# Optimization experiments

Measured on AMD Instinct MI355X. Metric: run time of the kernel, lower is better.

## Reference

```python
import jax, jax.numpy as jnp
import numpy as np

LSTM_IN = 125
LSTM_H = 125
MLP_D_H = 512
N = 512


def _lstm_scan(x, Wih, Whh, bih, bhh):
    # x: (N, LSTM_IN); PyTorch gate order: i, f, g, o
    H = LSTM_H
    def step(carry, xt):
        h, c = carry
        g = Wih @ xt + Whh @ h + bih + bhh  # (4H,)
        i = jax.nn.sigmoid(g[:H])
        f = jax.nn.sigmoid(g[H:2 * H])
        gg = jnp.tanh(g[2 * H:3 * H])
        o = jax.nn.sigmoid(g[3 * H:])
        c = f * c + i * gg
        h = o * jnp.tanh(c)
        return (h, c), h
    init = (jnp.zeros((H,), x.dtype), jnp.zeros((H,), x.dtype))
    _, hs = jax.lax.scan(step, init, x)
    return hs  # (N, H)


def setup_inputs() -> dict:
    key = jax.random.key(0)
    ks = jax.random.split(key, 14)
    s = 0.05
    d = {
        "sentence_emb": jax.random.normal(ks[0], (N, 1, LSTM_IN), jnp.float32),
        "Wih_f": jax.random.normal(ks[1], (4 * LSTM_H, LSTM_IN), jnp.float32) * s,
        "Whh_f": jax.random.normal(ks[2], (4 * LSTM_H, LSTM_H), jnp.float32) * s,
        "bih_f": jax.random.normal(ks[3], (4 * LSTM_H,), jnp.float32) * s,
        "bhh_f": jax.random.normal(ks[4], (4 * LSTM_H,), jnp.float32) * s,
        "Wih_b": jax.random.normal(ks[5], (4 * LSTM_H, LSTM_IN), jnp.float32) * s,
        "Whh_b": jax.random.normal(ks[6], (4 * LSTM_H, LSTM_H), jnp.float32) * s,
        "bih_b": jax.random.normal(ks[7], (4 * LSTM_H,), jnp.float32) * s,
        "bhh_b": jax.random.normal(ks[8], (4 * LSTM_H,), jnp.float32) * s,
        "W1": jax.random.normal(ks[9], (MLP_D_H, 4 * LSTM_H), jnp.float32) * s,
        "b1": jax.random.normal(ks[10], (MLP_D_H,), jnp.float32) * s,
        "W2": jax.random.normal(ks[11], (1, MLP_D_H), jnp.float32) * s,
        "b2": jax.random.normal(ks[12], (1,), jnp.float32) * s,
    }
    return d


def reference(sentence_emb, Wih_f, Whh_f, bih_f, bhh_f, Wih_b, Whh_b, bih_b, bhh_b, W1, b1, W2, b2):
    x = sentence_emb[:, 0, :]  # (N, 125), batch=1
    h_fwd = _lstm_scan(x, Wih_f, Whh_f, bih_f, bhh_f)           # (N, 125)
    h_bwd = _lstm_scan(x[::-1], Wih_b, Whh_b, bih_b, bhh_b)[::-1]  # (N, 125)
    h = jnp.concatenate([h_fwd, h_bwd], axis=-1)  # (N, 250)
    # output_mtx[i, j] = MLP(concat(h[j], h[i]))
    # Decompose first linear: W1 @ cat(h_j, h_i) = Wa @ h_j + Wb @ h_i
    D = h.shape[-1]
    Pa = h @ W1[:, :D].T   # (N, H): contribution of h_j
    Pb = h @ W1[:, D:].T   # (N, H): contribution of h_i
    hidden = jnp.tanh(Pb[:, None, :] + Pa[None, :, :] + b1)  # (N, N, H)
    out = hidden @ W2[0] + b2[0]  # (N, N)
    return out
```

## Files before the change

### kernel.cpp

```cpp
#include <hip/hip_runtime.h>

typedef __bf16 bf16_t;
typedef __bf16 bf16x8 __attribute__((ext_vector_type(8)));
typedef float f32x4 __attribute__((ext_vector_type(4)));
typedef int   int4v __attribute__((ext_vector_type(4)));

#define LOG2E 1.4426950408889634f

template<int CTRL>
__device__ __forceinline__ float qperm(float x) {
  return __builtin_bit_cast(float,
      __builtin_amdgcn_update_dpp(0, __builtin_bit_cast(int, x), CTRL, 0xF, 0xF, true));
}

__device__ __forceinline__ void lds_barrier() {
  asm volatile("s_waitcnt lgkmcnt(0)\n\ts_barrier" ::: "memory");
}

__global__ __launch_bounds__(256) void pre_kernel(
    const float* __restrict__ x,
    const float* __restrict__ Wih_f, const float* __restrict__ bih_f,
    const float* __restrict__ bhh_f,
    const float* __restrict__ Wih_b, const float* __restrict__ bih_b,
    const float* __restrict__ bhh_b,
    float* __restrict__ preT)
{
  const int dir = blockIdx.x >> 5;
  const int T   = blockIdx.x & 31;
  const float* __restrict__ Wih = dir ? Wih_b : Wih_f;
  const float* __restrict__ bih = dir ? bih_b : bih_f;
  const float* __restrict__ bhh = dir ? bhh_b : bhh_f;

  const int tid = threadIdx.x;
  const int wv  = tid >> 6;
  const int lane = tid & 63;
  const int q = lane >> 4, cc = lane & 15;

  const int r  = 16 * T + cc;
  const int na = r >> 2, pa = r & 3;
  const bool vld = (na < 125);
  const float* __restrict__ Wr = Wih + (vld ? (125 * pa + na) * 125 : 0);

  bf16x8 whi[4], wlo[4];
  #pragma unroll
  for (int ks = 0; ks < 4; ++ks) {
    #pragma unroll
    for (int j = 0; j < 8; ++j) {
      int k = 32 * ks + 8 * q + j;
      float wvv = (vld && k < 125) ? Wr[k] : 0.0f;
      bf16_t hi = (bf16_t)wvv;
      whi[ks][j] = hi;
      wlo[ks][j] = (bf16_t)(wvv - (float)hi);
    }
  }

  float bias[4];
  #pragma unroll
  for (int reg = 0; reg < 4; ++reg) {
    int ro = 16 * T + 4 * q + reg;
    int no = ro >> 2, po = ro & 3;
    bias[reg] = (no < 125) ? (bih[125 * po + no] + bhh[125 * po + no]) : 0.0f;
  }

  for (int i = 0; i < 8; ++i) {
    const int tt = 8 * wv + i;
    const int t  = 16 * tt + cc;
    const int trow = dir ? (511 - t) : t;
    const float* __restrict__ xr = x + trow * 125;

    f32x4 acc = (f32x4)0.0f;
    #pragma unroll
    for (int ks = 0; ks < 4; ++ks) {
      bf16x8 xhi, xlo;
      #pragma unroll
      for (int j = 0; j < 8; ++j) {
        int k = 32 * ks + 8 * q + j;
        float xv = (k < 125) ? xr[k] : 0.0f;
        bf16_t hi = (bf16_t)xv;
        xhi[j] = hi;
        xlo[j] = (bf16_t)(xv - (float)hi);
      }
      acc = __builtin_amdgcn_mfma_f32_16x16x32_bf16(whi[ks], xhi, acc, 0, 0, 0);
      acc = __builtin_amdgcn_mfma_f32_16x16x32_bf16(whi[ks], xlo, acc, 0, 0, 0);
      acc = __builtin_amdgcn_mfma_f32_16x16x32_bf16(wlo[ks], xhi, acc, 0, 0, 0);
    }
    #pragma unroll
    for (int reg = 0; reg < 4; ++reg) {
      int ro = 16 * T + 4 * q + reg;
      preT[dir * 262144 + ro * 512 + 16 * tt + cc] = acc[reg] + bias[reg];
    }
  }
}

__global__ __launch_bounds__(512) void lstm_kernel(
    const float* __restrict__ Whh_f, const float* __restrict__ Whh_b,
    const float* __restrict__ pre,
    bf16_t* __restrict__ h_all)
{
  const int dir = blockIdx.x;
  const float* __restrict__ Whh = dir ? Whh_b : Whh_f;

  const int tid  = threadIdx.x;
  const int lane = tid & 63;
  const int w    = tid >> 6;
  const int q    = lane >> 4;
  const int cc   = lane & 15;
  const int lt   = cc >> 2;
  const int p    = cc & 3;

  float wm = 0.0f;
  #pragma unroll
  for (int LT = 0; LT < 4; ++LT) {
    int rr = 16 * (4 * w + LT) + cc;
    int nn = rr >> 2, pp = rr & 3;
    if (nn < 125) {
      const float* __restrict__ Wrow = Whh + (125 * pp + nn) * 125;
      #pragma unroll
      for (int ks = 0; ks < 2; ++ks)
        #pragma unroll
        for (int jj = 0; jj < 16; ++jj) {
          int k = 64 * ks + 16 * q + jj;
          if (k < 125) wm = fmaxf(wm, fabsf(Wrow[k]));
        }
    }
  }
  #pragma unroll
  for (int off = 1; off < 64; off <<= 1)
    wm = fmaxf(wm, __shfl_xor(wm, off));
  __shared__ float wmx[8];
  if (lane == 0) wmx[w] = wm;
  __syncthreads();
  float wmax = wmx[0];
  #pragma unroll
  for (int u = 1; u < 8; ++u) wmax = fmaxf(wmax, wmx[u]);
  const float s_w  = 127.0f / wmax;
  const float invq = wmax / (127.0f * 127.0f);

  int4v afrag[4][2];
  #pragma unroll
  for (int LT = 0; LT < 4; ++LT) {
    int rr = 16 * (4 * w + LT) + cc;
    int nn = rr >> 2, pp = rr & 3;
    bool avld = (nn < 125);
    const float* __restrict__ Wrow = Whh + (avld ? (125 * pp + nn) * 125 : 0);
    #pragma unroll
    for (int ks = 0; ks < 2; ++ks) {
      int4v v;
      #pragma unroll
      for (int word = 0; word < 4; ++word) {
        int b = 0;
        #pragma unroll
        for (int byte = 0; byte < 4; ++byte) {
          int jj = 4 * word + byte;
          int k  = 64 * ks + 16 * q + jj;
          int qv = 0;
          if (avld && k < 125)
            qv = (int)__builtin_rintf(Wrow[k] * s_w);
          b |= (qv & 0xFF) << (8 * byte);
        }
        v[word] = b;
      }
      afrag[LT][ks] = v;
    }
  }

  __shared__ __align__(16) char hbuf[2][128];
  if (tid < 256) hbuf[tid >> 7][tid & 127] = 0;
  if (dir == 0) {
    #pragma unroll
    for (int u = 0; u < 6; ++u) h_all[tid * 256 + 250 + u] = (bf16_t)0.0f;
  }
  __syncthreads();

  const int   r_lane = 64 * w + 16 * lt + 4 * q + p;
  const int   nset   = 16 * w + 4 * lt + q;
  const float mult   = (p == 2) ? (-2.0f * LOG2E) : (-LOG2E);
  const float sA     = (p == 2) ? 2.0f : 1.0f;
  const float sB     = (p == 2) ? -1.0f : 0.0f;
  const float dscale = mult * invq;
  const float* __restrict__ preR = pre + dir * 262144 + r_lane * 512;
  float c = 0.0f;

  float4 pv_cur = *(const float4*)preR;

  for (int g = 0; g < 128; ++g) {
    float4 pv_nxt = make_float4(0.f, 0.f, 0.f, 0.f);
    if (g < 127) pv_nxt = *(const float4*)(preR + 4 * (g + 1));

    #pragma unroll
    for (int s4 = 0; s4 < 4; ++s4) {
      const int step = 4 * g + s4;
      const int cur  = s4 & 1, nxt = cur ^ 1;
      const float pv = (s4 == 0) ? pv_cur.x : (s4 == 1) ? pv_cur.y
                     : (s4 == 2) ? pv_cur.z : pv_cur.w;
      const float pvm = mult * pv;

      int4v b0 = *(const int4v*)&hbuf[cur][16 * q];
      int4v b1 = *(const int4v*)&hbuf[cur][64 + 16 * q];

      int4v acc[4];
      #pragma unroll
      for (int LT = 0; LT < 4; ++LT) {
        int4v a = (int4v)0;
        a = __builtin_amdgcn_mfma_i32_16x16x64_i8(afrag[LT][0], b0, a, 0, 0, 0);
        a = __builtin_amdgcn_mfma_i32_16x16x64_i8(afrag[LT][1], b1, a, 0, 0, 0);
        acc[LT] = a;
      }

      int gl[4];
      #pragma unroll
      for (int LT = 0; LT < 4; ++LT) {
        int a01 = (p & 1) ? acc[LT][1] : acc[LT][0];
        int a23 = (p & 1) ? acc[LT][3] : acc[LT][2];
        gl[LT] = (p & 2) ? a23 : a01;
      }
      int b01 = (lt & 1) ? gl[1] : gl[0];
      int b23 = (lt & 1) ? gl[3] : gl[2];
      int gsel = (lt & 2) ? b23 : b01;

      float gf  = (float)gsel;
      float xg  = fmaf(gf, dscale, pvm);
      float e   = __builtin_amdgcn_exp2f(xg);
      float y   = __builtin_amdgcn_rcpf(1.0f + e);
      float act = fmaf(y, sA, sB);

      float b_i = qperm<0x00>(act);
      float b_f = qperm<0x55>(act);
      float b_g = qperm<0xAA>(act);
      float b_o = qperm<0xFF>(act);
      c = fmaf(b_f, c, b_i * b_g);
      float e2 = __builtin_amdgcn_exp2f(-2.0f * LOG2E * c);
      float tc = fmaf(__builtin_amdgcn_rcpf(1.0f + e2), 2.0f, -1.0f);
      float h  = b_o * tc;

      if (p == 0) {
        int qh = (int)__builtin_rintf(h * 127.0f);
        hbuf[nxt][nset] = (char)qh;
        if (nset < 125) {
          int t_orig = dir ? (511 - step) : step;
          h_all[t_orig * 256 + dir * 125 + nset] = (bf16_t)h;
        }
      }
      lds_barrier();
    }
    pv_cur = pv_nxt;
  }
}

__global__ __launch_bounds__(256) void qgemm_kernel(
    const bf16_t* __restrict__ h_all,
    const float* __restrict__ W1,
    const float* __restrict__ b1,
    float* __restrict__ Qa,
    float* __restrict__ Qb)
{
  const int tid  = threadIdx.x;
  const int wv   = tid >> 6;
  const int lane = tid & 63;
  const int q    = lane >> 4, cc = lane & 15;
  const int bj   = blockIdx.x & 31;
  const int bm   = blockIdx.x >> 5;
  const int m    = bm * 64 + wv * 16 + cc;
  const int j0   = bj * 16;
  const int jA   = j0 + cc;

  const bool isB = (m >= 512);
  const int  row = isB ? (m - 512) : m;
  const int  cof = isB ? 250 : 0;

  f32x4 acc = (f32x4)0.0f;
  #pragma unroll
  for (int ks = 0; ks < 8; ++ks) {
    int kb = 32 * ks + 8 * q;
    bf16x8 a = *(const bf16x8*)&h_all[jA * 256 + kb];
    bf16x8 b;
    #pragma unroll
    for (int jj = 0; jj < 8; ++jj) {
      int k = kb + jj;
      float v = (k < 250) ? W1[row * 500 + cof + k] : 0.0f;
      b[jj] = (bf16_t)v;
    }
    acc = __builtin_amdgcn_mfma_f32_16x16x32_bf16(a, b, acc, 0, 0, 0);
  }

  const float C2 = 2.0f * LOG2E;
  #pragma unroll
  for (int reg = 0; reg < 4; ++reg) {
    int j = j0 + 4 * q + reg;
    float v = acc[reg];
    if (!isB) Qa[j * 512 + m] = C2 * v;
    else      Qb[j * 512 + (m - 512)] = C2 * (v + b1[m - 512]);
  }
}

__global__ __launch_bounds__(256) void outer_kernel(
    const float* __restrict__ Qa, const float* __restrict__ Qb,
    const float* __restrict__ W2, const float* __restrict__ b2,
    float* __restrict__ out)
{
  __shared__ float sa[2][32][33];
  __shared__ float sb[2][32][33];
  __shared__ float sw[2][32];

  const int tid = threadIdx.x;
  const int bi  = blockIdx.x >> 4, bjx = blockIdx.x & 15;
  const int i0  = bi * 32, j0 = bjx * 32;
  const int ii0 = (tid & 15) * 2;
  const int jj0 = (tid >> 4) * 2;
  const int ljj = tid & 31, kk4 = (tid >> 5) * 4;

  float accR[2][2] = {{0.0f, 0.0f}, {0.0f, 0.0f}};
  float wsum = 0.0f;

  for (int kc = 0; kc < 16; ++kc) {
    const int buf = kc & 1;
    const int k0  = kc * 32;
    float4 va = *(const float4*)&Qa[(j0 + ljj) * 512 + k0 + kk4];
    float4 vb = *(const float4*)&Qb[(i0 + ljj) * 512 + k0 + kk4];
    sa[buf][kk4 + 0][ljj] = va.x; sa[buf][kk4 + 1][ljj] = va.y;
    sa[buf][kk4 + 2][ljj] = va.z; sa[buf][kk4 + 3][ljj] = va.w;
    sb[buf][kk4 + 0][ljj] = vb.x; sb[buf][kk4 + 1][ljj] = vb.y;
    sb[buf][kk4 + 2][ljj] = vb.z; sb[buf][kk4 + 3][ljj] = vb.w;
    if (tid < 32) sw[buf][tid] = W2[k0 + tid];
    __syncthreads();

    #pragma unroll 4
    for (int kk = 0; kk < 32; ++kk) {
      float2 av = *(const float2*)&sa[buf][kk][jj0];
      float2 bv = *(const float2*)&sb[buf][kk][ii0];
      float wk = sw[buf][kk];
      wsum += wk;
      {
        float e = __builtin_amdgcn_exp2f(av.x + bv.x);
        accR[0][0] = fmaf(wk, __builtin_amdgcn_rcpf(1.0f + e), accR[0][0]);
      }
      {
        float e = __builtin_amdgcn_exp2f(av.y + bv.x);
        accR[0][1] = fmaf(wk, __builtin_amdgcn_rcpf(1.0f + e), accR[0][1]);
      }
      {
        float e = __builtin_amdgcn_exp2f(av.x + bv.y);
        accR[1][0] = fmaf(wk, __builtin_amdgcn_rcpf(1.0f + e), accR[1][0]);
      }
      {
        float e = __builtin_amdgcn_exp2f(av.y + bv.y);
        accR[1][1] = fmaf(wk, __builtin_amdgcn_rcpf(1.0f + e), accR[1][1]);
      }
    }
  }

  const float bb = b2[0];
  #pragma unroll
  for (int i2 = 0; i2 < 2; ++i2)
    #pragma unroll
    for (int j2 = 0; j2 < 2; ++j2)
      out[(i0 + ii0 + i2) * 512 + (j0 + jj0 + j2)] =
          wsum - 2.0f * accR[i2][j2] + bb;
}

extern "C" void kernel_launch(void* const* d_in, const int* in_sizes, int n_in,
                              void* d_out, int out_size, void* d_ws, size_t ws_size,
                              hipStream_t stream) {
  const float* emb   = (const float*)d_in[0];
  const float* Wih_f = (const float*)d_in[1];
  const float* Whh_f = (const float*)d_in[2];
  const float* bih_f = (const float*)d_in[3];
  const float* bhh_f = (const float*)d_in[4];
  const float* Wih_b = (const float*)d_in[5];
  const float* Whh_b = (const float*)d_in[6];
  const float* bih_b = (const float*)d_in[7];
  const float* bhh_b = (const float*)d_in[8];
  const float* W1    = (const float*)d_in[9];
  const float* b1    = (const float*)d_in[10];
  const float* W2    = (const float*)d_in[11];
  const float* b2    = (const float*)d_in[12];
  float* out = (float*)d_out;

  char* ws = (char*)d_ws;
  float*  pre   = (float*)ws;
  bf16_t* h_all = (bf16_t*)(ws + 2 * 1024 * 1024);
  float*  Qa    = (float*)(ws + 2 * 1024 * 1024 + 256 * 1024);
  float*  Qb    = Qa + 512 * 512;

  pre_kernel<<<64, 256, 0, stream>>>(emb, Wih_f, bih_f, bhh_f,
                                     Wih_b, bih_b, bhh_b, pre);
  lstm_kernel<<<2, 512, 0, stream>>>(Whh_f, Whh_b, pre, h_all);
  qgemm_kernel<<<512, 256, 0, stream>>>(h_all, W1, b1, Qa, Qb);
  outer_kernel<<<256, 256, 0, stream>>>(Qa, Qb, W2, b2, out);
}
```

Measured before the change: 336.3 us.

## Replace per-step int8 MFMA recurrent matvec with per-thread sdot4 dot products

```diff
diff --git a/kernel.cpp b/kernel.cpp
--- a/kernel.cpp
+++ b/kernel.cpp
@@ -16,6 +16,19 @@
 __device__ __forceinline__ void lds_barrier() {
   asm volatile("s_waitcnt lgkmcnt(0)\n\ts_barrier" ::: "memory");
 }
+
+#if __has_builtin(__builtin_amdgcn_sdot4)
+__device__ __forceinline__ int DOT4(int a, int b, int c) {
+  return __builtin_amdgcn_sdot4(a, b, c, false);
+}
+#else
+__device__ __forceinline__ int DOT4(int a, int b, int c) {
+  #pragma unroll
+  for (int i = 0; i < 4; ++i)
+    c += ((a << (24 - 8 * i)) >> 24) * ((b << (24 - 8 * i)) >> 24);
+  return c;
+}
+#endif
 
 __global__ __launch_bounds__(256) void pre_kernel(
     const float* __restrict__ x,
@@ -103,27 +116,23 @@
   const int tid  = threadIdx.x;
   const int lane = tid & 63;
   const int w    = tid >> 6;
-  const int q    = lane >> 4;
-  const int cc   = lane & 15;
-  const int lt   = cc >> 2;
-  const int p    = cc & 3;
-
-  float wm = 0.0f;
-  #pragma unroll
-  for (int LT = 0; LT < 4; ++LT) {
-    int rr = 16 * (4 * w + LT) + cc;
-    int nn = rr >> 2, pp = rr & 3;
-    if (nn < 125) {
-      const float* __restrict__ Wrow = Whh + (125 * pp + nn) * 125;
-      #pragma unroll
-      for (int ks = 0; ks < 2; ++ks)
-        #pragma unroll
-        for (int jj = 0; jj < 16; ++jj) {
-          int k = 64 * ks + 16 * q + jj;
-          if (k < 125) wm = fmaxf(wm, fabsf(Wrow[k]));
-        }
-    }
-  }
+  const int n    = tid >> 2;
+  const int p    = tid & 3;
+  const bool vld = (n < 125);
+  const float* __restrict__ Wrow = Whh + (vld ? (125 * p + n) * 125 : 0);
+
+  float m0 = 0.f, m1 = 0.f, m2 = 0.f, m3 = 0.f;
+  if (vld) {
+    #pragma unroll 4
+    for (int k = 0; k < 124; k += 4) {
+      m0 = fmaxf(m0, fabsf(Wrow[k + 0]));
+      m1 = fmaxf(m1, fabsf(Wrow[k + 1]));
+      m2 = fmaxf(m2, fabsf(Wrow[k + 2]));
+      m3 = fmaxf(m3, fabsf(Wrow[k + 3]));
+    }
+    m0 = fmaxf(m0, fabsf(Wrow[124]));
+  }
+  float wm = fmaxf(fmaxf(m0, m1), fmaxf(m2, m3));
   #pragma unroll
   for (int off = 1; off < 64; off <<= 1)
     wm = fmaxf(wm, __shfl_xor(wm, off));
@@ -136,49 +145,34 @@
   const float s_w  = 127.0f / wmax;
   const float invq = wmax / (127.0f * 127.0f);
 
-  int4v afrag[4][2];
-  #pragma unroll
-  for (int LT = 0; LT < 4; ++LT) {
-    int rr = 16 * (4 * w + LT) + cc;
-    int nn = rr >> 2, pp = rr & 3;
-    bool avld = (nn < 125);
-    const float* __restrict__ Wrow = Whh + (avld ? (125 * pp + nn) * 125 : 0);
-    #pragma unroll
-    for (int ks = 0; ks < 2; ++ks) {
-      int4v v;
-      #pragma unroll
-      for (int word = 0; word < 4; ++word) {
-        int b = 0;
-        #pragma unroll
-        for (int byte = 0; byte < 4; ++byte) {
-          int jj = 4 * word + byte;
-          int k  = 64 * ks + 16 * q + jj;
-          int qv = 0;
-          if (avld && k < 125)
-            qv = (int)__builtin_rintf(Wrow[k] * s_w);
-          b |= (qv & 0xFF) << (8 * byte);
-        }
-        v[word] = b;
-      }
-      afrag[LT][ks] = v;
-    }
+  int wq[32];
+  #pragma unroll
+  for (int word = 0; word < 32; ++word) {
+    int b = 0;
+    #pragma unroll
+    for (int byte = 0; byte < 4; ++byte) {
+      int k = 4 * word + byte;
+      int qv = 0;
+      if (vld && k < 125)
+        qv = (int)__builtin_rintf(Wrow[k] * s_w);
+      b |= (qv & 0xFF) << (8 * byte);
+    }
+    wq[word] = b;
   }
 
   __shared__ __align__(16) char hbuf[2][128];
-  if (tid < 256) hbuf[tid >> 7][tid & 127] = 0;
+  if (tid < 256) ((char*)hbuf)[tid] = 0;
   if (dir == 0) {
     #pragma unroll
     for (int u = 0; u < 6; ++u) h_all[tid * 256 + 250 + u] = (bf16_t)0.0f;
   }
   __syncthreads();
 
-  const int   r_lane = 64 * w + 16 * lt + 4 * q + p;
-  const int   nset   = 16 * w + 4 * lt + q;
   const float mult   = (p == 2) ? (-2.0f * LOG2E) : (-LOG2E);
   const float sA     = (p == 2) ? 2.0f : 1.0f;
   const float sB     = (p == 2) ? -1.0f : 0.0f;
   const float dscale = mult * invq;
-  const float* __restrict__ preR = pre + dir * 262144 + r_lane * 512;
+  const float* __restrict__ preR = pre + dir * 262144 + tid * 512;
   float c = 0.0f;
 
   float4 pv_cur = *(const float4*)preR;
@@ -195,30 +189,27 @@
                      : (s4 == 2) ? pv_cur.z : pv_cur.w;
       const float pvm = mult * pv;
 
-      int4v b0 = *(const int4v*)&hbuf[cur][16 * q];
-      int4v b1 = *(const int4v*)&hbuf[cur][64 + 16 * q];
-
-      int4v acc[4];
+      int hv[32];
       #pragma unroll
-      for (int LT = 0; LT < 4; ++LT) {
-        int4v a = (int4v)0;
-        a = __builtin_amdgcn_mfma_i32_16x16x64_i8(afrag[LT][0], b0, a, 0, 0, 0);
-        a = __builtin_amdgcn_mfma_i32_16x16x64_i8(afrag[LT][1], b1, a, 0, 0, 0);
-        acc[LT] = a;
-      }
-
-      int gl[4];
+      for (int j = 0; j < 8; ++j) {
+        int4v v = *(const int4v*)&hbuf[cur][16 * j];
+        hv[4 * j + 0] = v[0];
+        hv[4 * j + 1] = v[1];
+        hv[4 * j + 2] = v[2];
+        hv[4 * j + 3] = v[3];
+      }
+
+      int d0 = 0, d1 = 0, d2 = 0, d3 = 0;
       #pragma unroll
-      for (int LT = 0; LT < 4; ++LT) {
-        int a01 = (p & 1) ? acc[LT][1] : acc[LT][0];
-        int a23 = (p & 1) ? acc[LT][3] : acc[LT][2];
-        gl[LT] = (p & 2) ? a23 : a01;
-      }
-      int b01 = (lt & 1) ? gl[1] : gl[0];
-      int b23 = (lt & 1) ? gl[3] : gl[2];
-      int gsel = (lt & 2) ? b23 : b01;
-
-      float gf  = (float)gsel;
+      for (int j = 0; j < 8; ++j) {
+        d0 = DOT4(wq[4 * j + 0], hv[4 * j + 0], d0);
+        d1 = DOT4(wq[4 * j + 1], hv[4 * j + 1], d1);
+        d2 = DOT4(wq[4 * j + 2], hv[4 * j + 2], d2);
+        d3 = DOT4(wq[4 * j + 3], hv[4 * j + 3], d3);
+      }
+      const int D = (d0 + d1) + (d2 + d3);
+
+      float gf  = (float)D;
       float xg  = fmaf(gf, dscale, pvm);
       float e   = __builtin_amdgcn_exp2f(xg);
       float y   = __builtin_amdgcn_rcpf(1.0f + e);
@@ -235,10 +226,10 @@
 
       if (p == 0) {
         int qh = (int)__builtin_rintf(h * 127.0f);
-        hbuf[nxt][nset] = (char)qh;
-        if (nset < 125) {
+        hbuf[nxt][n] = (char)qh;
+        if (n < 125) {
           int t_orig = dir ? (511 - step) : step;
-          h_all[t_orig * 256 + dir * 125 + nset] = (bf16_t)h;
+          h_all[t_orig * 256 + dir * 125 + n] = (bf16_t)h;
         }
       }
       lds_barrier();
```

New measurement: 378.7 us. 12.6% more time.
